# Performance work log

Measured on AMD Instinct MI355X. Metric: run time of the kernel, lower is better.

The kernel has to match this reference:

```python
import jax, jax.numpy as jnp
import numpy as np

N_NODES = 100000
N_EDGES = 1600000
EPS = 1e-5  # nn.BatchNorm1d default eps


def setup_inputs() -> dict:
    key = jax.random.key(0)
    ks = jax.random.split(key, 6)
    x = jax.random.normal(ks[0], (N_NODES, 11), dtype=jnp.float32)
    edge_index = jax.random.randint(ks[1], (2, N_EDGES), 0, N_NODES, dtype=jnp.int64)
    edge_weight = jax.random.uniform(ks[2], (N_EDGES,), dtype=jnp.float32)
    W1 = jax.random.normal(ks[3], (11, 64), dtype=jnp.float32) * 0.3
    b1 = jnp.zeros((64,), dtype=jnp.float32)
    gamma = jnp.ones((64,), dtype=jnp.float32)
    beta = jnp.zeros((64,), dtype=jnp.float32)
    W2 = jax.random.normal(ks[4], (64, 128), dtype=jnp.float32) * 0.125
    b2 = jnp.zeros((128,), dtype=jnp.float32)
    return {"x": x, "edge_index": edge_index, "edge_weight": edge_weight,
            "W1": W1, "b1": b1, "gamma": gamma, "beta": beta, "W2": W2, "b2": b2}


def _gcn_conv(x, row, col, w, W, b, n_nodes):
    """PyG GCNConv: h = x @ W; symmetric-norm aggregate at col; + bias.
    row/col/w already include self loops (weight 1.0)."""
    h = x @ W  # [N, F_out]
    deg = jax.ops.segment_sum(w, col, num_segments=n_nodes)  # [N]
    dinv = jnp.where(deg > 0, jax.lax.rsqrt(jnp.maximum(deg, 1e-12)), 0.0)
    norm = dinv[row] * w * dinv[col]  # [E+N]
    msg = h[row] * norm[:, None]  # gather + scale, [E+N, F_out]
    out = jax.ops.segment_sum(msg, col, num_segments=n_nodes)  # scatter-add
    return out + b


def _batch_norm(x, gamma, beta):
    # training-mode BatchNorm1d over node dimension, biased variance
    mean = jnp.mean(x, axis=0)
    var = jnp.mean(jnp.square(x - mean), axis=0)
    return (x - mean) * jax.lax.rsqrt(var + EPS) * gamma + beta


def reference(x, edge_index, edge_weight, W1, b1, gamma, beta, W2, b2):
    n = x.shape[0]
    loops = jnp.arange(n, dtype=edge_index.dtype)
    row = jnp.concatenate([edge_index[0], loops])
    col = jnp.concatenate([edge_index[1], loops])
    w = jnp.concatenate([edge_weight, jnp.ones((n,), dtype=edge_weight.dtype)])

    h = _gcn_conv(x, row, col, w, W1, b1, n)
    h = _batch_norm(h, gamma, beta)
    h = jax.nn.relu(h)
    # dropout is identity at inference (deterministic baseline)
    out = _gcn_conv(h, row, col, w, W2, b2, n)
    return out
```

## Files before the change

### kernel.cpp

```cpp
#include <hip/hip_runtime.h>

#define F0 11
#define F1 64
#define F2 128
#define TN2 128

#define CHUNKS 64
#define BPR 12544
#define WPR (BPR / 2)
#define NBS 1024
#define NBKT (CHUNKS * 8 * 4)

__device__ __forceinline__ unsigned short f2bf(float v) {
  unsigned u = __float_as_uint(v);
  unsigned r = u + 0x7FFFu + ((u >> 16) & 1u);
  return (unsigned short)(r >> 16);
}
__device__ __forceinline__ float bf2f(unsigned short s) {
  return __uint_as_float(((unsigned)s) << 16);
}
__device__ __forceinline__ float bf2f_lo(unsigned v) {
  return __uint_as_float(v << 16);
}
__device__ __forceinline__ float bf2f_hi(unsigned v) {
  return __uint_as_float(v & 0xFFFF0000u);
}

__global__ void k_pad(const float* __restrict__ x, unsigned short* __restrict__ x16b, int n) {
  int i = blockIdx.x * blockDim.x + threadIdx.x;
  if (i >= n * 16) return;
  int r = i >> 4, f = i & 15;
  x16b[i] = (f < F0) ? f2bf(x[(size_t)r * F0 + f]) : (unsigned short)0;
}

__global__ __launch_bounds__(1024) void k_cnt8(const int* __restrict__ col,
                                               int* __restrict__ bcnt, int E, int CE) {
  __shared__ int scnt[16][8];
  int bid = blockIdx.x;
  int c = bid >> 2, q = bid & 3;
  int e0 = c * CE, e1 = min(E, e0 + CE);
  int S = (CE + 3) >> 2;
  int s0 = e0 + q * S, s1 = min(e1, s0 + S);
  int t = threadIdx.x, wv = t >> 6, lane = t & 63;
  int cr[8] = {0, 0, 0, 0, 0, 0, 0, 0};
  for (int e = s0 + t; e < s1; e += 1024) {
    int r = col[e] / BPR;
#pragma unroll
    for (int rr = 0; rr < 8; rr++) cr[rr] += (r == rr) ? 1 : 0;
  }
#pragma unroll
  for (int rr = 0; rr < 8; rr++) {
    int v = cr[rr];
#pragma unroll
    for (int d = 32; d > 0; d >>= 1) v += __shfl_down(v, d);
    if (lane == 0) scnt[wv][rr] = v;
  }
  __syncthreads();
  if (t < 8) {
    int s = 0;
    for (int i = 0; i < 16; i++) s += scnt[i][t];
    bcnt[(c * 8 + t) * 4 + q] = s;
  }
}

__global__ void k_scan8(const int* __restrict__ bcnt, int* __restrict__ boff) {
  __shared__ int s[1024];
  int t = threadIdx.x;
  int v0 = bcnt[2 * t], v1 = bcnt[2 * t + 1];
  int pv = v0 + v1;
  s[t] = pv;
  __syncthreads();
  for (int d = 1; d < 1024; d <<= 1) {
    int x = (t >= d) ? s[t - d] : 0;
    __syncthreads();
    s[t] += x;
    __syncthreads();
  }
  int ex = s[t] - pv;
  boff[2 * t] = ex;
  boff[2 * t + 1] = ex + v0;
  if (t == 1023) boff[2048] = s[1023];
}

__global__ __launch_bounds__(1024) void k_scatter(const int* __restrict__ col,
                                                  const int* __restrict__ row,
                                                  const float* __restrict__ w,
                                                  const int* __restrict__ boff,
                                                  unsigned short* __restrict__ bloc,
                                                  uint2* __restrict__ brw, int E, int CE) {
  __shared__ int cur[8];
  int bid = blockIdx.x;
  int c = bid >> 2, q = bid & 3;
  int t = threadIdx.x;
  if (t < 8) cur[t] = boff[(c * 8 + t) * 4 + q];
  __syncthreads();
  int e0 = c * CE, e1 = min(E, e0 + CE);
  int S = (CE + 3) >> 2;
  int s0 = e0 + q * S, s1 = min(e1, s0 + S);
  for (int e = s0 + t; e < s1; e += 1024) {
    int b = col[e];
    int r = b / BPR;
    int pos = atomicAdd(&cur[r], 1);
    bloc[pos] = (unsigned short)(b - r * BPR);
    brw[pos] = make_uint2((unsigned)row[e], __float_as_uint(w[e]));
  }
}

__global__ __launch_bounds__(1024) void k_hist2(const unsigned short* __restrict__ bloc,
                                                const int* __restrict__ boff,
                                                unsigned* __restrict__ partial, int ranges) {
  __shared__ unsigned lds[WPR];
  int r = blockIdx.x % ranges;
  int c = blockIdx.x / ranges;
  int t = threadIdx.x;
  for (int i = t; i < WPR; i += 1024) lds[i] = 0;
  __syncthreads();
  int s0 = boff[(c * 8 + r) * 4], s1 = boff[(c * 8 + r) * 4 + 4];
  for (int i = s0 + t; i < s1; i += 1024) {
    int local = bloc[i];
    atomicAdd(&lds[local >> 1], 1u << (16 * (local & 1)));
  }
  __syncthreads();
  unsigned* dst = partial + ((size_t)r * CHUNKS + c) * WPR;
  for (int i = t; i < WPR; i += 1024) dst[i] = lds[i];
}

__global__ void k_colprefix(const unsigned* __restrict__ partial,
                            unsigned short* __restrict__ rel,
                            int* __restrict__ cnt, int N, int npad) {
  int bin = blockIdx.x * blockDim.x + threadIdx.x;
  if (bin >= N) return;
  int r = bin / BPR, local = bin % BPR;
  int word = local >> 1, sh = 16 * (local & 1);
  const unsigned* p = partial + (size_t)r * CHUNKS * WPR + word;
  unsigned acc = 0;
  for (int c = 0; c < CHUNKS; c++) {
    unsigned v = (p[(size_t)c * WPR] >> sh) & 0xFFFFu;
    rel[(size_t)c * npad + bin] = (unsigned short)acc;
    acc += v;
  }
  cnt[bin] = (int)acc;
}

__global__ void k_scan1(const int* __restrict__ cnt, int* __restrict__ offs,
                        int* __restrict__ bsum, int n) {
  __shared__ int s[1024];
  int tid = threadIdx.x;
  int i = blockIdx.x * 1024 + tid;
  int v = (i < n) ? cnt[i] : 0;
  s[tid] = v;
  __syncthreads();
  for (int d = 1; d < 1024; d <<= 1) {
    int t = (tid >= d) ? s[tid - d] : 0;
    __syncthreads();
    s[tid] += t;
    __syncthreads();
  }
  if (i < n) offs[i] = s[tid] - v;
  if (tid == 1023) bsum[blockIdx.x] = s[1023];
}

__global__ void k_scan2(int* __restrict__ bsum, int nb) {
  __shared__ int s[256];
  __shared__ int carry;
  int t = threadIdx.x;
  if (t == 0) carry = 0;
  __syncthreads();
  for (int base = 0; base < nb; base += 256) {
    int v = (base + t < nb) ? bsum[base + t] : 0;
    s[t] = v;
    __syncthreads();
    for (int d = 1; d < 256; d <<= 1) {
      int x = (t >= d) ? s[t - d] : 0;
      __syncthreads();
      s[t] += x;
      __syncthreads();
    }
    int total = s[255];
    if (base + t < nb) bsum[base + t] = carry + s[t] - v;
    __syncthreads();
    if (t == 0) carry += total;
    __syncthreads();
  }
}

__global__ void k_scan3(int* __restrict__ offs, const int* __restrict__ bsum,
                        int n, int total) {
  int i = blockIdx.x * 1024 + threadIdx.x;
  if (i < n) offs[i] += bsum[blockIdx.x];
  if (i == 0) offs[n] = total;
}

__global__ __launch_bounds__(1024) void k_fill2(const unsigned short* __restrict__ bloc,
                                                const uint2* __restrict__ brw,
                                                const int* __restrict__ boff,
                                                const int* __restrict__ offs,
                                                const unsigned short* __restrict__ rel,
                                                uint2* __restrict__ csr8,
                                                int N, int npad, int ranges) {
  __shared__ unsigned cur[WPR];
  int r = blockIdx.x % ranges;
  int c = blockIdx.x / ranges;
  int lo = r * BPR;
  int hi = min(N, lo + BPR);
  int t = threadIdx.x;
  const unsigned* rsrc = (const unsigned*)(rel + (size_t)c * npad + lo);
  int nw = (hi - lo + 1) >> 1;
  for (int i = t; i < nw; i += 1024) cur[i] = rsrc[i];
  __syncthreads();
  int s0 = boff[(c * 8 + r) * 4], s1 = boff[(c * 8 + r) * 4 + 4];
  for (int i = s0 + t; i < s1; i += 1024) {
    int local = bloc[i];
    int sh = 16 * (local & 1);
    unsigned old = atomicAdd(&cur[local >> 1], 1u << sh);
    unsigned myrel = (old >> sh) & 0xFFFFu;
    int pos = offs[lo + local] + (int)myrel;
    csr8[pos] = brw[i];
  }
}

__global__ void k_deg2(const uint2* __restrict__ csr8, const int* __restrict__ offs,
                       float* __restrict__ dinv, int n) {
  int wid = (blockIdx.x * blockDim.x + threadIdx.x) >> 6;
  int lane = threadIdx.x & 63;
  if (wid >= n) return;
  int s = offs[wid], e = offs[wid + 1];
  float acc = 0.f;
  for (int k = s + lane; k < e; k += 64) acc += __uint_as_float(csr8[k].y);
#pragma unroll
  for (int d = 32; d > 0; d >>= 1) acc += __shfl_down(acc, d);
  if (lane == 0) dinv[wid] = rsqrtf(1.0f + acc);
}

__global__ void k_norm(uint2* __restrict__ csr8, const float* __restrict__ dinv, int E) {
  int i = blockIdx.x * blockDim.x + threadIdx.x;
  if (i >= E) return;
  uint2 v = csr8[i];
  csr8[i].y = __float_as_uint(dinv[v.x] * __uint_as_float(v.y));
}

__global__ void k_agg1g(const unsigned short* __restrict__ x16b, const int* __restrict__ offs,
                        const uint2* __restrict__ csr8, const float* __restrict__ dinv,
                        const float* __restrict__ W1, const float* __restrict__ b1,
                        unsigned short* __restrict__ h, int n) {
  __shared__ float Ws[F0 * F1];
  __shared__ float bs[F1];
  __shared__ unsigned s_soff[4][64];
  __shared__ float    s_nrm[4][64];
  int t = threadIdx.x;
  for (int i = t; i < F0 * F1; i += 256) Ws[i] = W1[i];
  if (t < F1) bs[t] = b1[t];
  __syncthreads();
  int wv = t >> 6;
  int lane = t & 63;
  int wid = (blockIdx.x * blockDim.x + t) >> 6;
  if (wid >= n) return;
  int g = lane >> 4, f = lane & 15;
  float di = dinv[wid];
  float a0 = (g == 0) ? di * bf2f(x16b[(size_t)wid * 16 + f]) : 0.f;
  float a1 = 0.f, a2 = 0.f, a3 = 0.f;
  int s = offs[wid], e = offs[wid + 1];
  for (int base = s; base < e; base += 64) {
    int m = e - base; if (m > 64) m = 64;
    if (lane < m) {
      uint2 v = csr8[base + lane];
      s_soff[wv][lane] = v.x * 16u;
      s_nrm[wv][lane] = __uint_as_float(v.y);
    } else {
      s_soff[wv][lane] = 0u;
      s_nrm[wv][lane] = 0.f;
    }
    int mp = (m + 15) & ~15;
    for (int jb = 0; jb < mp; jb += 16) {
      unsigned o0 = s_soff[wv][jb + g],      o1 = s_soff[wv][jb + 4 + g];
      unsigned o2 = s_soff[wv][jb + 8 + g],  o3 = s_soff[wv][jb + 12 + g];
      float    m0 = s_nrm[wv][jb + g],       m1 = s_nrm[wv][jb + 4 + g];
      float    m2 = s_nrm[wv][jb + 8 + g],   m3 = s_nrm[wv][jb + 12 + g];
      a0 += m0 * bf2f(x16b[(size_t)o0 + f]);
      a1 += m1 * bf2f(x16b[(size_t)o1 + f]);
      a2 += m2 * bf2f(x16b[(size_t)o2 + f]);
      a3 += m3 * bf2f(x16b[(size_t)o3 + f]);
    }
  }
  float acc = (a0 + a1) + (a2 + a3);
  acc += __shfl_xor(acc, 16);
  acc += __shfl_xor(acc, 32);
  float av = di * acc;
  float o = bs[lane];
#pragma unroll
  for (int k = 0; k < F0; k++) o += __shfl(av, k) * Ws[k * F1 + lane];
  h[(size_t)wid * F1 + lane] = f2bf(o);
}

__global__ void k_bn_stats(const unsigned short* __restrict__ h, float2* __restrict__ pbn,
                           int total4) {
  int t = threadIdx.x;
  int idx = blockIdx.x * blockDim.x + t;
  int stride = gridDim.x * blockDim.x;
  const unsigned long long* hp = (const unsigned long long*)h;
  float s0 = 0, s1 = 0, s2 = 0, s3 = 0, q0 = 0, q1 = 0, q2 = 0, q3 = 0;
  for (int i = idx; i < total4; i += stride) {
    unsigned long long vv = hp[i];
    unsigned vx = (unsigned)vv, vy = (unsigned)(vv >> 32);
    float a = bf2f_lo(vx), b = bf2f_hi(vx);
    float c = bf2f_lo(vy), d = bf2f_hi(vy);
    s0 += a; q0 += a * a;
    s1 += b; q1 += b * b;
    s2 += c; q2 += c * c;
    s3 += d; q3 += d * d;
  }
  __shared__ float ss[256][4], qq[256][4];
  ss[t][0] = s0; ss[t][1] = s1; ss[t][2] = s2; ss[t][3] = s3;
  qq[t][0] = q0; qq[t][1] = q1; qq[t][2] = q2; qq[t][3] = q3;
  __syncthreads();
  if (t < 64) {
    int o = t >> 2, sub = t & 3;
    float S = 0.f, Q = 0.f;
#pragma unroll
    for (int i = 0; i < 16; i++) {
      S += ss[o + 16 * i][sub];
      Q += qq[o + 16 * i][sub];
    }
    pbn[(size_t)blockIdx.x * 64 + t] = make_float2(S, Q);
  }
}

__global__ void k_bn_mid(const float2* __restrict__ pbn, float2* __restrict__ pbn2) {
  __shared__ float sS[4][64], sQ[4][64];
  int t = threadIdx.x;
  int f = t & 63, g = t >> 6;
  int b0 = blockIdx.x * 16;
  float S = 0.f, Q = 0.f;
  for (int b = b0 + g; b < b0 + 16; b += 4) {
    float2 v = pbn[(size_t)b * 64 + f];
    S += v.x; Q += v.y;
  }
  sS[g][f] = S; sQ[g][f] = Q;
  __syncthreads();
  if (t < 64)
    pbn2[(size_t)blockIdx.x * 64 + t] =
        make_float2(sS[0][t] + sS[1][t] + sS[2][t] + sS[3][t],
                    sQ[0][t] + sQ[1][t] + sQ[2][t] + sQ[3][t]);
}

__global__ void k_bn_final(const float2* __restrict__ pbn2, const float* __restrict__ gamma,
                           const float* __restrict__ beta, float* __restrict__ scalef,
                           float* __restrict__ shiftf, int n) {
  __shared__ double sS[4][64], sQ[4][64];
  int t = threadIdx.x;
  int f = t & 63, g = t >> 6;
  double S = 0.0, Q = 0.0;
  for (int b = g; b < 64; b += 4) {
    float2 v = pbn2[(size_t)b * 64 + f];
    S += v.x; Q += v.y;
  }
  sS[g][f] = S; sQ[g][f] = Q;
  __syncthreads();
  if (t < 64) {
    double SS = sS[0][t] + sS[1][t] + sS[2][t] + sS[3][t];
    double QQ = sQ[0][t] + sQ[1][t] + sQ[2][t] + sQ[3][t];
    double mean = SS / (double)n;
    double var = QQ / (double)n - mean * mean;
    if (var < 0.0) var = 0.0;
    float scale = gamma[t] * (float)(1.0 / sqrt(var + 1e-5));
    scalef[t] = scale;
    shiftf[t] = beta[t] - (float)mean * scale;
  }
}

__global__ void k_agg2(const unsigned short* __restrict__ h, const int* __restrict__ offs,
                       const uint2* __restrict__ csr8, const float* __restrict__ dinv,
                       const float* __restrict__ scalef, const float* __restrict__ shiftf,
                       float* __restrict__ agg2, int n) {
  __shared__ unsigned s_soff[4][64];
  __shared__ float    s_nrm[4][64];
  int t = threadIdx.x;
  int wv = t >> 6;
  int lane = t & 63;
  int wid = (blockIdx.x * blockDim.x + t) >> 6;
  if (wid >= n) return;
  float sc = scalef[lane], sf = shiftf[lane];
  float di = dinv[wid];
  float a0 = di * fmaxf(fmaf(bf2f(h[(size_t)wid * F1 + lane]), sc, sf), 0.f);
  float a1 = 0.f, a2 = 0.f, a3 = 0.f, a4 = 0.f, a5 = 0.f, a6 = 0.f, a7 = 0.f;
  int s = offs[wid], e = offs[wid + 1];
  for (int base = s; base < e; base += 64) {
    int m = e - base; if (m > 64) m = 64;
    if (lane < m) {
      uint2 v = csr8[base + lane];
      s_soff[wv][lane] = v.x * 64u;
      s_nrm[wv][lane] = __uint_as_float(v.y);
    } else {
      s_soff[wv][lane] = 0u;
      s_nrm[wv][lane] = 0.f;
    }
    int mp = (m + 7) & ~7;
    for (int j = 0; j < mp; j += 8) {
      unsigned o0 = s_soff[wv][j + 0], o1 = s_soff[wv][j + 1];
      unsigned o2 = s_soff[wv][j + 2], o3 = s_soff[wv][j + 3];
      unsigned o4 = s_soff[wv][j + 4], o5 = s_soff[wv][j + 5];
      unsigned o6 = s_soff[wv][j + 6], o7 = s_soff[wv][j + 7];
      float m0 = s_nrm[wv][j + 0], m1 = s_nrm[wv][j + 1];
      float m2 = s_nrm[wv][j + 2], m3 = s_nrm[wv][j + 3];
      float m4 = s_nrm[wv][j + 4], m5 = s_nrm[wv][j + 5];
      float m6 = s_nrm[wv][j + 6], m7 = s_nrm[wv][j + 7];
      a0 += m0 * fmaxf(fmaf(bf2f(h[(size_t)o0 + lane]), sc, sf), 0.f);
      a1 += m1 * fmaxf(fmaf(bf2f(h[(size_t)o1 + lane]), sc, sf), 0.f);
      a2 += m2 * fmaxf(fmaf(bf2f(h[(size_t)o2 + lane]), sc, sf), 0.f);
      a3 += m3 * fmaxf(fmaf(bf2f(h[(size_t)o3 + lane]), sc, sf), 0.f);
      a4 += m4 * fmaxf(fmaf(bf2f(h[(size_t)o4 + lane]), sc, sf), 0.f);
      a5 += m5 * fmaxf(fmaf(bf2f(h[(size_t)o5 + lane]), sc, sf), 0.f);
      a6 += m6 * fmaxf(fmaf(bf2f(h[(size_t)o6 + lane]), sc, sf), 0.f);
      a7 += m7 * fmaxf(fmaf(bf2f(h[(size_t)o7 + lane]), sc, sf), 0.f);
    }
  }
  agg2[(size_t)wid * F1 + lane] =
      di * (((a0 + a1) + (a2 + a3)) + ((a4 + a5) + (a6 + a7)));
}

__global__ __launch_bounds__(256) void k_gemm2(const float* __restrict__ agg2,
                                               const float* __restrict__ W2,
                                               const float* __restrict__ b2,
                                               float* __restrict__ out, int n) {
  __shared__ float Ws[F1 * F2];
  __shared__ float As[F1][TN2];
  int t = threadIdx.x;
  for (int i = t; i < F1 * F2 / 4; i += 256) ((float4*)Ws)[i] = ((const float4*)W2)[i];
  int nb = blockIdx.x * TN2;
  int node = t & 127;
  int kh = (t >> 7) * 32;
  int gnode = nb + node;
  if (gnode < n) {
    const float4* src = (const float4*)(agg2 + (size_t)gnode * F1 + kh);
#pragma unroll
    for (int j = 0; j < 8; j++) {
      float4 v = src[j];
      As[kh + j * 4 + 0][node] = v.x;
      As[kh + j * 4 + 1][node] = v.y;
      As[kh + j * 4 + 2][node] = v.z;
      As[kh + j * 4 + 3][node] = v.w;
    }
  } else {
#pragma unroll
    for (int j = 0; j < 8; j++) {
      As[kh + j * 4 + 0][node] = 0.f;
      As[kh + j * 4 + 1][node] = 0.f;
      As[kh + j * 4 + 2][node] = 0.f;
      As[kh + j * 4 + 3][node] = 0.f;
    }
  }
  __syncthreads();

  int f0 = (t & 15) * 8;
  int n0 = (t >> 4) * 8;
  float acc[8][8];
  float bv[8];
#pragma unroll
  for (int j = 0; j < 8; j++) bv[j] = b2[f0 + j];
#pragma unroll
  for (int i = 0; i < 8; i++)
#pragma unroll
    for (int j = 0; j < 8; j++) acc[i][j] = bv[j];

#pragma unroll 4
  for (int k = 0; k < F1; k++) {
    float4 a0 = *(const float4*)&As[k][n0];
    float4 a1 = *(const float4*)&As[k][n0 + 4];
    float4 w0 = *(const float4*)&Ws[k * F2 + f0];
    float4 w1 = *(const float4*)&Ws[k * F2 + f0 + 4];
    float a[8] = {a0.x, a0.y, a0.z, a0.w, a1.x, a1.y, a1.z, a1.w};
    float w[8] = {w0.x, w0.y, w0.z, w0.w, w1.x, w1.y, w1.z, w1.w};
#pragma unroll
    for (int i = 0; i < 8; i++)
#pragma unroll
      for (int j = 0; j < 8; j++) acc[i][j] += a[i] * w[j];
  }

#pragma unroll
  for (int i = 0; i < 8; i++) {
    int gi = nb + n0 + i;
    if (gi < n) {
      float4 o0 = {acc[i][0], acc[i][1], acc[i][2], acc[i][3]};
      float4 o1 = {acc[i][4], acc[i][5], acc[i][6], acc[i][7]};
      *(float4*)&out[(size_t)gi * F2 + f0] = o0;
      *(float4*)&out[(size_t)gi * F2 + f0 + 4] = o1;
    }
  }
}

extern "C" void kernel_launch(void* const* d_in, const int* in_sizes, int n_in,
                              void* d_out, int out_size, void* d_ws, size_t ws_size,
                              hipStream_t stream) {
  const float* x     = (const float*)d_in[0];
  const int*   ei    = (const int*)d_in[1];
  const float* ew    = (const float*)d_in[2];
  const float* W1    = (const float*)d_in[3];
  const float* b1    = (const float*)d_in[4];
  const float* gamma = (const float*)d_in[5];
  const float* beta  = (const float*)d_in[6];
  const float* W2    = (const float*)d_in[7];
  const float* b2    = (const float*)d_in[8];
  float* out = (float*)d_out;

  int N = in_sizes[0] / F0;
  int E = in_sizes[1] / 2;
  const int* row = ei;
  const int* col = ei + E;
  if (N <= 0) return;

  int CE = (E + CHUNKS - 1) / CHUNKS;
  int RANGES = (N + BPR - 1) / BPR;
  int npad = RANGES * BPR;

  char* p = (char*)d_ws;
  auto alloc = [&](size_t bytes) -> void* {
    void* r = (void*)p;
    p += (bytes + 255) & ~(size_t)255;
    return r;
  };
  size_t partial_bytes = ((size_t)RANGES * CHUNKS * WPR * 4 + 255) & ~(size_t)255;
  size_t rel_bytes     = (size_t)CHUNKS * npad * 2;
  size_t h_bytes       = (size_t)N * F1 * 2;
  size_t region_bytes  = partial_bytes + rel_bytes;
  if (h_bytes > region_bytes) region_bytes = h_bytes;

  float*          dinv    = (float*)alloc((size_t)N * 4);
  int*            cnt     = (int*)alloc((size_t)N * 4);
  int*            offs    = (int*)alloc((size_t)(N + 1) * 4);
  int             NB      = (N + 1023) / 1024;
  int*            bsum    = (int*)alloc((size_t)NB * 4);
  uint2*          csr8    = (uint2*)alloc((size_t)E * 8);
  char*           region  = (char*)alloc(region_bytes);
  unsigned*       partial = (unsigned*)region;
  unsigned short* rel     = (unsigned short*)(region + partial_bytes);
  unsigned short* h       = (unsigned short*)region;
  unsigned short* x16b    = (unsigned short*)alloc((size_t)N * 16 * 2);
  float*          agg2    = (float*)alloc((size_t)N * F1 * 4);
  float2*         pbn     = (float2*)alloc((size_t)NBS * 64 * 8);
  float2*         pbn2    = (float2*)alloc((size_t)64 * 64 * 8);
  float*          scalef  = (float*)alloc(64 * 4);
  float*          shiftf  = (float*)alloc(64 * 4);
  int*            bcnt    = (int*)alloc((size_t)NBKT * 4);
  int*            boff    = (int*)alloc((size_t)(NBKT + 1) * 4);
  size_t bloc_bytes = (((size_t)E * 2) + 255) & ~(size_t)255;
  unsigned short* bloc = (unsigned short*)agg2;
  uint2*          brw  = (uint2*)((char*)agg2 + bloc_bytes);
  (void)ws_size; (void)n_in; (void)out_size;

  int bW  = (N + 3) / 4;
  int bG2 = (N + TN2 - 1) / TN2;
  int gRC = CHUNKS * RANGES;

  k_pad<<<(N * 16 + 255) / 256, 256, 0, stream>>>(x, x16b, N);
  k_cnt8<<<CHUNKS * 4, 1024, 0, stream>>>(col, bcnt, E, CE);
  k_scan8<<<1, 1024, 0, stream>>>(bcnt, boff);
  k_scatter<<<CHUNKS * 4, 1024, 0, stream>>>(col, row, ew, boff, bloc, brw, E, CE);
  k_hist2<<<gRC, 1024, 0, stream>>>(bloc, boff, partial, RANGES);
  k_colprefix<<<(N + 255) / 256, 256, 0, stream>>>(partial, rel, cnt, N, npad);
  k_scan1<<<NB, 1024, 0, stream>>>(cnt, offs, bsum, N);
  k_scan2<<<1, 256, 0, stream>>>(bsum, NB);
  k_scan3<<<NB, 1024, 0, stream>>>(offs, bsum, N, E);
  k_fill2<<<gRC, 1024, 0, stream>>>(bloc, brw, boff, offs, rel, csr8, N, npad, RANGES);
  k_deg2<<<bW, 256, 0, stream>>>(csr8, offs, dinv, N);
  k_norm<<<(E + 255) / 256, 256, 0, stream>>>(csr8, dinv, E);
  k_agg1g<<<bW, 256, 0, stream>>>(x16b, offs, csr8, dinv, W1, b1, h, N);
  k_bn_stats<<<NBS, 256, 0, stream>>>(h, pbn, N * F1 / 4);
  k_bn_mid<<<64, 256, 0, stream>>>(pbn, pbn2);
  k_bn_final<<<1, 256, 0, stream>>>(pbn2, gamma, beta, scalef, shiftf, N);
  k_agg2<<<bW, 256, 0, stream>>>(h, offs, csr8, dinv, scalef, shiftf, agg2, N);
  k_gemm2<<<bG2, 256, 0, stream>>>(agg2, W2, b2, out, N);
}
```

Measured before the change: 235.9 us.

## Use edge-balanced block aggregation with LDS segmented accumulation and fused BN stats

Both aggregation kernels now give each block a group of 64 destination nodes and split that block's combined edge range evenly across threads or waves. Each thread keeps a run-length sum per destination and flushes it to shared-memory accumulators with atomics, which evens out load across nodes with different degrees. To support this, the local destination index is packed into the upper bits of the CSR source word. Layer-1 aggregation also computes the BN partial sums, removing the separate stats pass. A new k_hn pass writes a BN+ReLU-normalized bf16 copy of h so layer 2 gathers ready values, at the cost of an extra buffer and a full pass over h.

```diff
diff --git a/kernel.cpp b/kernel.cpp
--- a/kernel.cpp
+++ b/kernel.cpp
@@ -8,8 +8,8 @@
 #define CHUNKS 64
 #define BPR 12544
 #define WPR (BPR / 2)
-#define NBS 1024
 #define NBKT (CHUNKS * 8 * 4)
+#define NN1 64
 
 __device__ __forceinline__ unsigned short f2bf(float v) {
   unsigned u = __float_as_uint(v);
@@ -19,12 +19,8 @@
 __device__ __forceinline__ float bf2f(unsigned short s) {
   return __uint_as_float(((unsigned)s) << 16);
 }
-__device__ __forceinline__ float bf2f_lo(unsigned v) {
-  return __uint_as_float(v << 16);
-}
-__device__ __forceinline__ float bf2f_hi(unsigned v) {
-  return __uint_as_float(v & 0xFFFF0000u);
-}
+__device__ __forceinline__ float bf2f_lo(unsigned v) { return __uint_as_float(v << 16); }
+__device__ __forceinline__ float bf2f_hi(unsigned v) { return __uint_as_float(v & 0xFFFF0000u); }
 
 __global__ void k_pad(const float* __restrict__ x, unsigned short* __restrict__ x16b, int n) {
   int i = blockIdx.x * blockDim.x + threadIdx.x;
@@ -215,7 +211,8 @@
     unsigned old = atomicAdd(&cur[local >> 1], 1u << sh);
     unsigned myrel = (old >> sh) & 0xFFFFu;
     int pos = offs[lo + local] + (int)myrel;
-    csr8[pos] = brw[i];
+    uint2 b = brw[i];
+    csr8[pos] = make_uint2(b.x | ((unsigned)local << 17), b.y);
   }
 }
 
@@ -236,102 +233,104 @@
   int i = blockIdx.x * blockDim.x + threadIdx.x;
   if (i >= E) return;
   uint2 v = csr8[i];
-  csr8[i].y = __float_as_uint(dinv[v.x] * __uint_as_float(v.y));
-}
-
-__global__ void k_agg1g(const unsigned short* __restrict__ x16b, const int* __restrict__ offs,
-                        const uint2* __restrict__ csr8, const float* __restrict__ dinv,
-                        const float* __restrict__ W1, const float* __restrict__ b1,
-                        unsigned short* __restrict__ h, int n) {
+  csr8[i].y = __float_as_uint(dinv[v.x & 0x1FFFFu] * __uint_as_float(v.y));
+}
+
+__global__ __launch_bounds__(256) void k_agg1e(const unsigned short* __restrict__ x16b,
+                                               const int* __restrict__ offs,
+                                               const uint2* __restrict__ csr8,
+                                               const float* __restrict__ dinv,
+                                               const float* __restrict__ W1,
+                                               const float* __restrict__ b1,
+                                               unsigned short* __restrict__ h,
+                                               float2* __restrict__ pbn, int N) {
   __shared__ float Ws[F0 * F1];
   __shared__ float bs[F1];
-  __shared__ unsigned s_soff[4][64];
-  __shared__ float    s_nrm[4][64];
-  int t = threadIdx.x;
+  __shared__ float sacc[NN1 * 16];
+  __shared__ unsigned short sx[NN1 * 16];
+  __shared__ float sdinv[NN1];
+  __shared__ float sS[4][64], sQ[4][64];
+  int t = threadIdx.x;
+  int bid = blockIdx.x;
+  int n0 = bid * NN1;
+  int nn = min(NN1, N - n0);
+  int lbase = n0 - (n0 / BPR) * BPR;
   for (int i = t; i < F0 * F1; i += 256) Ws[i] = W1[i];
   if (t < F1) bs[t] = b1[t];
-  __syncthreads();
-  int wv = t >> 6;
-  int lane = t & 63;
-  int wid = (blockIdx.x * blockDim.x + t) >> 6;
-  if (wid >= n) return;
-  int g = lane >> 4, f = lane & 15;
-  float di = dinv[wid];
-  float a0 = (g == 0) ? di * bf2f(x16b[(size_t)wid * 16 + f]) : 0.f;
-  float a1 = 0.f, a2 = 0.f, a3 = 0.f;
-  int s = offs[wid], e = offs[wid + 1];
-  for (int base = s; base < e; base += 64) {
-    int m = e - base; if (m > 64) m = 64;
-    if (lane < m) {
-      uint2 v = csr8[base + lane];
-      s_soff[wv][lane] = v.x * 16u;
-      s_nrm[wv][lane] = __uint_as_float(v.y);
-    } else {
-      s_soff[wv][lane] = 0u;
-      s_nrm[wv][lane] = 0.f;
-    }
-    int mp = (m + 15) & ~15;
-    for (int jb = 0; jb < mp; jb += 16) {
-      unsigned o0 = s_soff[wv][jb + g],      o1 = s_soff[wv][jb + 4 + g];
-      unsigned o2 = s_soff[wv][jb + 8 + g],  o3 = s_soff[wv][jb + 12 + g];
-      float    m0 = s_nrm[wv][jb + g],       m1 = s_nrm[wv][jb + 4 + g];
-      float    m2 = s_nrm[wv][jb + 8 + g],   m3 = s_nrm[wv][jb + 12 + g];
-      a0 += m0 * bf2f(x16b[(size_t)o0 + f]);
-      a1 += m1 * bf2f(x16b[(size_t)o1 + f]);
-      a2 += m2 * bf2f(x16b[(size_t)o2 + f]);
-      a3 += m3 * bf2f(x16b[(size_t)o3 + f]);
-    }
-  }
-  float acc = (a0 + a1) + (a2 + a3);
-  acc += __shfl_xor(acc, 16);
-  acc += __shfl_xor(acc, 32);
-  float av = di * acc;
-  float o = bs[lane];
-#pragma unroll
-  for (int k = 0; k < F0; k++) o += __shfl(av, k) * Ws[k * F1 + lane];
-  h[(size_t)wid * F1 + lane] = f2bf(o);
-}
-
-__global__ void k_bn_stats(const unsigned short* __restrict__ h, float2* __restrict__ pbn,
-                           int total4) {
-  int t = threadIdx.x;
-  int idx = blockIdx.x * blockDim.x + t;
-  int stride = gridDim.x * blockDim.x;
-  const unsigned long long* hp = (const unsigned long long*)h;
-  float s0 = 0, s1 = 0, s2 = 0, s3 = 0, q0 = 0, q1 = 0, q2 = 0, q3 = 0;
-  for (int i = idx; i < total4; i += stride) {
-    unsigned long long vv = hp[i];
-    unsigned vx = (unsigned)vv, vy = (unsigned)(vv >> 32);
-    float a = bf2f_lo(vx), b = bf2f_hi(vx);
-    float c = bf2f_lo(vy), d = bf2f_hi(vy);
-    s0 += a; q0 += a * a;
-    s1 += b; q1 += b * b;
-    s2 += c; q2 += c * c;
-    s3 += d; q3 += d * d;
-  }
-  __shared__ float ss[256][4], qq[256][4];
-  ss[t][0] = s0; ss[t][1] = s1; ss[t][2] = s2; ss[t][3] = s3;
-  qq[t][0] = q0; qq[t][1] = q1; qq[t][2] = q2; qq[t][3] = q3;
-  __syncthreads();
-  if (t < 64) {
-    int o = t >> 2, sub = t & 3;
-    float S = 0.f, Q = 0.f;
-#pragma unroll
-    for (int i = 0; i < 16; i++) {
-      S += ss[o + 16 * i][sub];
-      Q += qq[o + 16 * i][sub];
-    }
-    pbn[(size_t)blockIdx.x * 64 + t] = make_float2(S, Q);
-  }
-}
-
-__global__ void k_bn_mid(const float2* __restrict__ pbn, float2* __restrict__ pbn2) {
+  ((uint2*)sx)[t] = ((const uint2*)(x16b + (size_t)n0 * 16))[t];
+  if (t < NN1) sdinv[t] = (t < nn) ? dinv[n0 + t] : 0.f;
+  for (int i = t; i < NN1 * 16; i += 256) sacc[i] = 0.f;
+  __syncthreads();
+  int ebase = offs[n0], eend = offs[n0 + nn];
+  int slot = t >> 4, f = t & 15;
+  int nsub = (eend - ebase + 15) >> 4;
+  int gs = ebase + slot * nsub;
+  int ge = min(eend, gs + nsub);
+  float sum = 0.f;
+  int cid = -1;
+  int e = gs;
+  for (; e + 4 <= ge; e += 4) {
+    uint2 v0 = csr8[e], v1 = csr8[e + 1], v2 = csr8[e + 2], v3 = csr8[e + 3];
+    int i0 = (int)(v0.x >> 17) - lbase, i1 = (int)(v1.x >> 17) - lbase;
+    int i2 = (int)(v2.x >> 17) - lbase, i3 = (int)(v3.x >> 17) - lbase;
+    float c0 = __uint_as_float(v0.y) * bf2f(x16b[(size_t)(v0.x & 0x1FFFFu) * 16 + f]);
+    float c1 = __uint_as_float(v1.y) * bf2f(x16b[(size_t)(v1.x & 0x1FFFFu) * 16 + f]);
+    float c2 = __uint_as_float(v2.y) * bf2f(x16b[(size_t)(v2.x & 0x1FFFFu) * 16 + f]);
+    float c3 = __uint_as_float(v3.y) * bf2f(x16b[(size_t)(v3.x & 0x1FFFFu) * 16 + f]);
+    bool sm;
+    sm = (i0 == cid); if (!sm && cid >= 0) atomicAdd(&sacc[cid * 16 + f], sum);
+    sum = sm ? sum + c0 : c0; cid = i0;
+    sm = (i1 == cid); if (!sm) atomicAdd(&sacc[cid * 16 + f], sum);
+    sum = sm ? sum + c1 : c1; cid = i1;
+    sm = (i2 == cid); if (!sm) atomicAdd(&sacc[cid * 16 + f], sum);
+    sum = sm ? sum + c2 : c2; cid = i2;
+    sm = (i3 == cid); if (!sm) atomicAdd(&sacc[cid * 16 + f], sum);
+    sum = sm ? sum + c3 : c3; cid = i3;
+  }
+  for (; e < ge; e++) {
+    uint2 v0 = csr8[e];
+    int i0 = (int)(v0.x >> 17) - lbase;
+    float c0 = __uint_as_float(v0.y) * bf2f(x16b[(size_t)(v0.x & 0x1FFFFu) * 16 + f]);
+    bool sm = (i0 == cid);
+    if (!sm && cid >= 0) atomicAdd(&sacc[cid * 16 + f], sum);
+    sum = sm ? sum + c0 : c0; cid = i0;
+  }
+  if (cid >= 0) atomicAdd(&sacc[cid * 16 + f], sum);
+  __syncthreads();
+  for (int i = t; i < NN1 * 16; i += 256) {
+    float di = sdinv[i >> 4];
+    sacc[i] = di * (sacc[i] + di * bf2f(sx[i]));
+  }
+  __syncthreads();
+  int ff = t & 63, wv = t >> 6;
+  float S = 0.f, Q = 0.f;
+  for (int i = 0; i < 16; i++) {
+    int nd = wv + 4 * i;
+    if (nd < nn) {
+      float o = bs[ff];
+#pragma unroll
+      for (int k = 0; k < F0; k++) o += sacc[nd * 16 + k] * Ws[k * F1 + ff];
+      h[(size_t)(n0 + nd) * F1 + ff] = f2bf(o);
+      S += o; Q += o * o;
+    }
+  }
+  sS[wv][ff] = S; sQ[wv][ff] = Q;
+  __syncthreads();
+  if (t < 64)
+    pbn[(size_t)bid * 64 + t] =
+        make_float2(sS[0][t] + sS[1][t] + sS[2][t] + sS[3][t],
+                    sQ[0][t] + sQ[1][t] + sQ[2][t] + sQ[3][t]);
+}
+
+__global__ void k_bn_mid(const float2* __restrict__ pbn, float2* __restrict__ pbn2, int nrows) {
   __shared__ float sS[4][64], sQ[4][64];
   int t = threadIdx.x;
   int f = t & 63, g = t >> 6;
-  int b0 = blockIdx.x * 16;
+  int rpb = (nrows + 63) / 64;
+  int b0 = blockIdx.x * rpb;
+  int bend = min(nrows, b0 + rpb);
   float S = 0.f, Q = 0.f;
-  for (int b = b0 + g; b < b0 + 16; b += 4) {
+  for (int b = b0 + g; b < bend; b += 4) {
     float2 v = pbn[(size_t)b * 64 + f];
     S += v.x; Q += v.y;
   }
@@ -368,54 +367,91 @@
   }
 }
 
-__global__ void k_agg2(const unsigned short* __restrict__ h, const int* __restrict__ offs,
-                       const uint2* __restrict__ csr8, const float* __restrict__ dinv,
-                       const float* __restrict__ scalef, const float* __restrict__ shiftf,
-                       float* __restrict__ agg2, int n) {
-  __shared__ unsigned s_soff[4][64];
-  __shared__ float    s_nrm[4][64];
-  int t = threadIdx.x;
-  int wv = t >> 6;
-  int lane = t & 63;
-  int wid = (blockIdx.x * blockDim.x + t) >> 6;
-  if (wid >= n) return;
-  float sc = scalef[lane], sf = shiftf[lane];
-  float di = dinv[wid];
-  float a0 = di * fmaxf(fmaf(bf2f(h[(size_t)wid * F1 + lane]), sc, sf), 0.f);
-  float a1 = 0.f, a2 = 0.f, a3 = 0.f, a4 = 0.f, a5 = 0.f, a6 = 0.f, a7 = 0.f;
-  int s = offs[wid], e = offs[wid + 1];
-  for (int base = s; base < e; base += 64) {
-    int m = e - base; if (m > 64) m = 64;
-    if (lane < m) {
-      uint2 v = csr8[base + lane];
-      s_soff[wv][lane] = v.x * 64u;
-      s_nrm[wv][lane] = __uint_as_float(v.y);
-    } else {
-      s_soff[wv][lane] = 0u;
-      s_nrm[wv][lane] = 0.f;
-    }
-    int mp = (m + 7) & ~7;
-    for (int j = 0; j < mp; j += 8) {
-      unsigned o0 = s_soff[wv][j + 0], o1 = s_soff[wv][j + 1];
-      unsigned o2 = s_soff[wv][j + 2], o3 = s_soff[wv][j + 3];
-      unsigned o4 = s_soff[wv][j + 4], o5 = s_soff[wv][j + 5];
-      unsigned o6 = s_soff[wv][j + 6], o7 = s_soff[wv][j + 7];
-      float m0 = s_nrm[wv][j + 0], m1 = s_nrm[wv][j + 1];
-      float m2 = s_nrm[wv][j + 2], m3 = s_nrm[wv][j + 3];
-      float m4 = s_nrm[wv][j + 4], m5 = s_nrm[wv][j + 5];
-      float m6 = s_nrm[wv][j + 6], m7 = s_nrm[wv][j + 7];
-      a0 += m0 * fmaxf(fmaf(bf2f(h[(size_t)o0 + lane]), sc, sf), 0.f);
-      a1 += m1 * fmaxf(fmaf(bf2f(h[(size_t)o1 + lane]), sc, sf), 0.f);
-      a2 += m2 * fmaxf(fmaf(bf2f(h[(size_t)o2 + lane]), sc, sf), 0.f);
-      a3 += m3 * fmaxf(fmaf(bf2f(h[(size_t)o3 + lane]), sc, sf), 0.f);
-      a4 += m4 * fmaxf(fmaf(bf2f(h[(size_t)o4 + lane]), sc, sf), 0.f);
-      a5 += m5 * fmaxf(fmaf(bf2f(h[(size_t)o5 + lane]), sc, sf), 0.f);
-      a6 += m6 * fmaxf(fmaf(bf2f(h[(size_t)o6 + lane]), sc, sf), 0.f);
-      a7 += m7 * fmaxf(fmaf(bf2f(h[(size_t)o7 + lane]), sc, sf), 0.f);
-    }
-  }
-  agg2[(size_t)wid * F1 + lane] =
-      di * (((a0 + a1) + (a2 + a3)) + ((a4 + a5) + (a6 + a7)));
+__global__ void k_hn(const unsigned short* __restrict__ h, const float* __restrict__ scalef,
+                     const float* __restrict__ shiftf, unsigned short* __restrict__ hn,
+                     int total4) {
+  __shared__ float ssc[64], ssf[64];
+  int t = threadIdx.x;
+  if (t < 64) { ssc[t] = scalef[t]; ssf[t] = shiftf[t]; }
+  __syncthreads();
+  int idx = blockIdx.x * blockDim.x + t;
+  int stride = gridDim.x * blockDim.x;
+  const unsigned long long* hp = (const unsigned long long*)h;
+  unsigned long long* hnp = (unsigned long long*)hn;
+  for (int i = idx; i < total4; i += stride) {
+    unsigned long long vv = hp[i];
+    int f0 = (i * 4) & 63;
+    float a = fmaxf(fmaf(bf2f_lo((unsigned)vv), ssc[f0 + 0], ssf[f0 + 0]), 0.f);
+    float b = fmaxf(fmaf(bf2f_hi((unsigned)vv), ssc[f0 + 1], ssf[f0 + 1]), 0.f);
+    float c = fmaxf(fmaf(bf2f_lo((unsigned)(vv >> 32)), ssc[f0 + 2], ssf[f0 + 2]), 0.f);
+    float d = fmaxf(fmaf(bf2f_hi((unsigned)(vv >> 32)), ssc[f0 + 3], ssf[f0 + 3]), 0.f);
+    hnp[i] = (unsigned long long)f2bf(a) | ((unsigned long long)f2bf(b) << 16) |
+             ((unsigned long long)f2bf(c) << 32) | ((unsigned long long)f2bf(d) << 48);
+  }
+}
+
+__global__ __launch_bounds__(256) void k_agg2e(const unsigned short* __restrict__ hn,
+                                               const int* __restrict__ offs,
+                                               const uint2* __restrict__ csr8,
+                                               const float* __restrict__ dinv,
+                                               float* __restrict__ agg2, int N) {
+  __shared__ float sacc[NN1 * F1];
+  __shared__ float sdinv[NN1];
+  int t = threadIdx.x;
+  int bid = blockIdx.x;
+  int n0 = bid * NN1;
+  int nn = min(NN1, N - n0);
+  int lbase = n0 - (n0 / BPR) * BPR;
+  int lane = t & 63, wv = t >> 6;
+  if (t < NN1) sdinv[t] = (t < nn) ? dinv[n0 + t] : 0.f;
+  for (int i = t; i < NN1 * F1; i += 256) sacc[i] = 0.f;
+  __syncthreads();
+  int ebase = offs[n0], eend = offs[n0 + nn];
+  int nsub = (eend - ebase + 3) >> 2;
+  int gs = ebase + wv * nsub;
+  int ge = min(eend, gs + nsub);
+  float sum = 0.f;
+  int cid = -1;
+  int e = gs;
+  for (; e + 8 <= ge; e += 8) {
+    uint2 v[8];
+#pragma unroll
+    for (int j = 0; j < 8; j++) v[j] = csr8[e + j];
+    float c[8];
+    int idx[8];
+#pragma unroll
+    for (int j = 0; j < 8; j++) {
+      idx[j] = (int)(v[j].x >> 17) - lbase;
+      c[j] = __uint_as_float(v[j].y) *
+             bf2f(hn[(size_t)(v[j].x & 0x1FFFFu) * F1 + lane]);
+    }
+#pragma unroll
+    for (int j = 0; j < 8; j++) {
+      bool sm = (idx[j] == cid);
+      if (!sm && cid >= 0) atomicAdd(&sacc[cid * F1 + lane], sum);
+      sum = sm ? sum + c[j] : c[j];
+      cid = idx[j];
+    }
+  }
+  for (; e < ge; e++) {
+    uint2 v0 = csr8[e];
+    int i0 = (int)(v0.x >> 17) - lbase;
+    float c0 = __uint_as_float(v0.y) * bf2f(hn[(size_t)(v0.x & 0x1FFFFu) * F1 + lane]);
+    bool sm = (i0 == cid);
+    if (!sm && cid >= 0) atomicAdd(&sacc[cid * F1 + lane], sum);
+    sum = sm ? sum + c0 : c0;
+    cid = i0;
+  }
+  if (cid >= 0) atomicAdd(&sacc[cid * F1 + lane], sum);
+  __syncthreads();
+  for (int i = 0; i < 16; i++) {
+    int nd = wv + 4 * i;
+    if (nd < nn) {
+      float di = sdinv[nd];
+      float self = bf2f(hn[(size_t)(n0 + nd) * F1 + lane]);
+      agg2[(size_t)(n0 + nd) * F1 + lane] = di * (sacc[nd * F1 + lane] + di * self);
+    }
+  }
 }
 
 __global__ __launch_bounds__(256) void k_gemm2(const float* __restrict__ agg2,
@@ -511,6 +547,7 @@
   int CE = (E + CHUNKS - 1) / CHUNKS;
   int RANGES = (N + BPR - 1) / BPR;
   int npad = RANGES * BPR;
+  int NBLK = (N + NN1 - 1) / NN1;
 
   char* p = (char*)d_ws;
   auto alloc = [&](size_t bytes) -> void* {
@@ -535,8 +572,9 @@
   unsigned short* rel     = (unsigned short*)(region + partial_bytes);
   unsigned short* h       = (unsigned short*)region;
   unsigned short* x16b    = (unsigned short*)alloc((size_t)N * 16 * 2);
+  unsigned short* hn      = (unsigned short*)alloc((size_t)N * F1 * 2);
   float*          agg2    = (float*)alloc((size_t)N * F1 * 4);
-  float2*         pbn     = (float2*)alloc((size_t)NBS * 64 * 8);
+  float2*         pbn     = (float2*)alloc((size_t)NBLK * 64 * 8);
   float2*         pbn2    = (float2*)alloc((size_t)64 * 64 * 8);
   float*          scalef  = (float*)alloc(64 * 4);
   float*          shiftf  = (float*)alloc(64 * 4);
@@ -563,10 +601,10 @@
   k_fill2<<<gRC, 1024, 0, stream>>>(bloc, brw, boff, offs, rel, csr8, N, npad, RANGES);
   k_deg2<<<bW, 256, 0, stream>>>(csr8, offs, dinv, N);
   k_norm<<<(E + 255) / 256, 256, 0, stream>>>(csr8, dinv, E);
-  k_agg1g<<<bW, 256, 0, stream>>>(x16b, offs, csr8, dinv, W1, b1, h, N);
-  k_bn_stats<<<NBS, 256, 0, stream>>>(h, pbn, N * F1 / 4);
-  k_bn_mid<<<64, 256, 0, stream>>>(pbn, pbn2);
+  k_agg1e<<<NBLK, 256, 0, stream>>>(x16b, offs, csr8, dinv, W1, b1, h, pbn, N);
+  k_bn_mid<<<64, 256, 0, stream>>>(pbn, pbn2, NBLK);
   k_bn_final<<<1, 256, 0, stream>>>(pbn2, gamma, beta, scalef, shiftf, N);
-  k_agg2<<<bW, 256, 0, stream>>>(h, offs, csr8, dinv, scalef, shiftf, agg2, N);
+  k_hn<<<2048, 256, 0, stream>>>(h, scalef, shiftf, hn, N * F1 / 4);
+  k_agg2e<<<NBLK, 256, 0, stream>>>(hn, offs, csr8, dinv, agg2, N);
   k_gemm2<<<bG2, 256, 0, stream>>>(agg2, W2, b2, out, N);
 }
```

Measured after the change: 246.1 us. 4.3% more time.
